# Performance work log

Hardware: AMD Instinct MI355X
Metric: run time of the kernel (lower is better)

Reference implementation:

```python
import jax, jax.numpy as jnp
import numpy as np

DECAY = 0.999
EPS = 1e-05
COMMITMENT_COST = 0.25
M, D = 1024, 256
B, H, W = 32, 32, 32


def setup_inputs() -> dict:
    key = jax.random.key(0)
    k1, k2 = jax.random.split(key)
    init_bound = 1.0 / M
    x = jax.random.normal(k1, (B, H, W, D), dtype=jnp.float32)
    embedding = jax.random.uniform(k2, (M, D), dtype=jnp.float32,
                                   minval=-init_bound, maxval=init_bound)
    ema_count = jnp.zeros((M,), dtype=jnp.float32)
    ema_weight = embedding  # buffer initialized as embedding.clone()
    return {"x": x, "embedding": embedding, "ema_count": ema_count,
            "ema_weight": ema_weight}


def reference(x, embedding, ema_count, ema_weight):
    Mn, Dn = embedding.shape
    x_flat = jax.lax.stop_gradient(x).reshape(-1, Dn)          # [N, D]
    N = x_flat.shape[0]

    # (-cdist)^2 == squared euclidean distance; argmin is the same.
    x_sq = jnp.sum(x_flat * x_flat, axis=-1, keepdims=True)    # [N, 1]
    e_sq = jnp.sum(embedding * embedding, axis=-1)             # [M]
    distances = x_sq - 2.0 * (x_flat @ embedding.T) + e_sq[None, :]  # [N, M]
    indices = jnp.argmin(distances, axis=-1)                   # [N]

    quantized = embedding[indices].reshape(x.shape)            # gather

    # one-hot column sums == scatter-add of ones; encodings.T @ x_flat == scatter-add rows
    counts = jnp.zeros((Mn,), x.dtype).at[indices].add(1.0)    # [M]
    dw = jnp.zeros((Mn, Dn), x.dtype).at[indices].add(x_flat)  # [M, D]

    new_count = DECAY * ema_count + (1.0 - DECAY) * counts
    n = jnp.sum(new_count)
    new_count = (new_count + EPS) / (n + Mn * EPS) * n
    new_weight = DECAY * ema_weight + (1.0 - DECAY) * dw
    new_embedding = new_weight / new_count[:, None]

    codebook_loss = jnp.mean((jax.lax.stop_gradient(x) - quantized) ** 2)
    e_latent_loss = jnp.mean((x - jax.lax.stop_gradient(quantized)) ** 2)
    commitment_loss = COMMITMENT_COST * e_latent_loss

    quantized_st = x + jax.lax.stop_gradient(quantized - x)    # straight-through

    avg_probs = counts / N
    perplexity = jnp.exp(-jnp.sum(avg_probs * jnp.log(avg_probs + 1e-10)))

    return (quantized_st, commitment_loss, codebook_loss, perplexity,
            new_embedding, new_count, new_weight)
```

## Files before the change

### kernel.cpp

```cpp
#include <hip/hip_runtime.h>
#include <cfloat>
#include <math.h>

#define N_TOK 32768
#define DIM   256
#define MCODE 1024

typedef unsigned short u16;
typedef unsigned long long u64;
typedef __attribute__((ext_vector_type(8))) _Float16 h16x8;
typedef __attribute__((ext_vector_type(4))) float f32x4;

constexpr float DECAY_ = 0.999f;
constexpr float OMD_   = (float)(1.0 - 0.999);
constexpr float EPS_   = 1e-5f;
constexpr float MEPS_  = (float)(1024 * 1e-5);

constexpr int WS_EH   = 0;
constexpr int WS_ESQ  = 262144;
constexpr int WS_CNTI = 263168;
constexpr int WS_BI   = 264192;
constexpr int WS_LP   = 296960;
constexpr int WS_KEY  = 299008;

constexpr int OUT_Q        = 0;
constexpr int OUT_COMMIT   = 8388608;
constexpr int OUT_CODEBOOK = 8388609;
constexpr int OUT_PERP     = 8388610;
constexpr int OUT_NE       = 8388611;
constexpr int OUT_NC       = 8650755;
constexpr int OUT_NW       = 8651779;

static __device__ __forceinline__ void gl2lds16(const u16* g, char* l) {
    __builtin_amdgcn_global_load_lds(
        (const __attribute__((address_space(1))) unsigned int*)g,
        (__attribute__((address_space(3))) unsigned int*)l, 16, 0, 0);
}
static __device__ __forceinline__ unsigned fmap(float f) {
    unsigned u = __float_as_uint(f);
    return (u & 0x80000000u) ? ~u : (u | 0x80000000u);
}

static __device__ __forceinline__ void load_row8(const float* __restrict__ src,
                                                 int wave_id, int lane,
                                                 float* vv, size_t* o) {
    int rb = wave_id >> 6, kc = (wave_id >> 3) & 7, t = wave_id & 7;
    int row = rb * 128 + t * 16 + (lane & 15);
    int k   = kc * 32 + (lane >> 4) * 8;
    const float* s = &src[row * DIM + k];
    float4 v0 = *(const float4*)s, v1 = *(const float4*)(s + 4);
    vv[0]=v0.x; vv[1]=v0.y; vv[2]=v0.z; vv[3]=v0.w;
    vv[4]=v1.x; vv[5]=v1.y; vv[6]=v1.z; vv[7]=v1.w;
    *o = (size_t)wave_id * 512 + lane * 8;
}
static __device__ __forceinline__ void pack_wave_h16(const float* __restrict__ src,
                                                     u16* __restrict__ dst,
                                                     int wave_id, int lane,
                                                     float scale) {
    float vv[8]; size_t o;
    load_row8(src, wave_id, lane, vv, &o);
    h16x8 hv;
#pragma unroll
    for (int j = 0; j < 8; ++j) hv[j] = (_Float16)(vv[j] * scale);
    *(h16x8*)&dst[o] = hv;
}

__global__ __launch_bounds__(256) void vq_setup(const float* __restrict__ x,
                                                const float* __restrict__ emb,
                                                u16* __restrict__ xh,
                                                u16* __restrict__ eh,
                                                float* __restrict__ esq,
                                                u64* __restrict__ keys,
                                                int* __restrict__ cnti) {
    const int b = blockIdx.x, tid = threadIdx.x;
    const int lane = tid & 63, w = tid >> 6;
    if (b < 4096) { pack_wave_h16(x, xh, b * 4 + w, lane, 1.0f); return; }
    const int p = b - 4096;
    if (p < 128) {
        pack_wave_h16(emb, eh, p * 4 + w, lane, 1024.0f);
    } else if (p < 384) {
        int c = (p - 128) * 4 + w;
        float4 v = *(const float4*)&emb[c * DIM + lane * 4];
        float s = v.x * v.x + v.y * v.y + v.z * v.z + v.w * v.w;
#pragma unroll
        for (int off = 32; off; off >>= 1) s += __shfl_xor(s, off, 64);
        if (lane == 0) esq[c] = s;
    } else if (p < 512) {
        keys[(p - 384) * 256 + tid] = ~0ULL;
    } else {
#pragma unroll
        for (int i = 0; i < 4; ++i) cnti[i * 256 + tid] = 0;
    }
}

__global__ __launch_bounds__(256) void vq_scores_mfma(const u16* __restrict__ xh,
                                                      const u16* __restrict__ eh,
                                                      const float* __restrict__ esq,
                                                      u64* __restrict__ keys) {
    __shared__ __align__(16) char smem[33792];
    const int tid  = threadIdx.x;
    const int lane = tid & 63, w = tid >> 6;
    const int wm = w & 1, wn = w >> 1;
    const int raw = blockIdx.x;
    const int rb = (raw >> 6) * 8 + (raw & 7);
    const int cs = (raw >> 3) & 7;

    const u16* gb0 = xh + (size_t)rb * 32768;
    const u16* gb1 = eh + (size_t)cs * 32768;

    auto STAGE = [&](int KC, char* base) {
#pragma unroll
        for (int j = 0; j < 4; ++j) {
            int t = w * 4 + j;
            int arr = t >> 3, slot = t & 7;
            const u16* g = (arr == 0 ? gb0 : gb1)
                           + KC * 4096 + slot * 512 + lane * 8;
            gl2lds16(g, base + arr * 8192 + slot * 1024);
        }
    };

    f32x4 acc[4][4];
#pragma unroll
    for (int i = 0; i < 4; ++i)
#pragma unroll
        for (int j = 0; j < 4; ++j) acc[i][j] = (f32x4)0.f;

    STAGE(0, smem);
    __syncthreads();

    for (int kc = 0; kc < 8; ++kc) {
        char* cur = smem + (kc & 1) * 16384;
        char* nxt = smem + ((kc + 1) & 1) * 16384;
        if (kc < 7) STAGE(kc + 1, nxt);

        const h16x8* Ah = (const h16x8*)cur;
        const h16x8* Bh = (const h16x8*)(cur + 8192);
        h16x8 ah[4];
#pragma unroll
        for (int tm = 0; tm < 4; ++tm)
            ah[tm] = Ah[(wm * 4 + tm) * 64 + lane];
#pragma unroll
        for (int tn = 0; tn < 4; ++tn) {
            h16x8 bh = Bh[(wn * 4 + tn) * 64 + lane];
#pragma unroll
            for (int tm = 0; tm < 4; ++tm) {
                acc[tm][tn] = __builtin_amdgcn_mfma_f32_16x16x32_f16(ah[tm], bh, acc[tm][tn], 0, 0, 0);
            }
        }
        __syncthreads();
    }

    float* cv = (float*)smem;
    int*   ci = (int*)(smem + 16896);
    const int ln = lane & 15, quad = lane >> 4;
#pragma unroll
    for (int tm = 0; tm < 4; ++tm) {
        float bv[4];
        int   bi[4];
#pragma unroll
        for (int r = 0; r < 4; ++r) { bv[r] = FLT_MAX; bi[r] = 0; }
#pragma unroll
        for (int tn = 0; tn < 4; ++tn) {
            int c = cs * 128 + wn * 64 + tn * 16 + ln;
            float ec = esq[c];
#pragma unroll
            for (int r = 0; r < 4; ++r) {
                float d = fmaf(-0.001953125f, acc[tm][tn][r], ec);
                if (d < bv[r]) { bv[r] = d; bi[r] = c; }
            }
        }
        int row0 = wm * 64 + tm * 16 + quad * 4;
        int slot = wn * 16 + ln;
#pragma unroll
        for (int r = 0; r < 4; ++r) {
            cv[(row0 + r) * 33 + slot] = bv[r];
            ci[(row0 + r) * 33 + slot] = bi[r];
        }
    }
    __syncthreads();
    if (tid < 128) {
        float bv = cv[tid * 33];
        int   bi = ci[tid * 33];
#pragma unroll
        for (int s = 1; s < 32; ++s) {
            float v = cv[tid * 33 + s];
            int  ix = ci[tid * 33 + s];
            if (v < bv || (v == bv && ix < bi)) { bv = v; bi = ix; }
        }
        u64 key = ((u64)fmap(bv) << 32) | (unsigned)bi;
        atomicMin(&keys[rb * 128 + tid], key);
    }
}

__global__ __launch_bounds__(256) void vq_quant(const float* __restrict__ x,
                                                const float* __restrict__ emb,
                                                const u64* __restrict__ keys,
                                                float* __restrict__ outq,
                                                int* __restrict__ cnti,
                                                int* __restrict__ bi_arr,
                                                float* __restrict__ lpart) {
    const int tid = threadIdx.x, lane = tid & 63, w = tid >> 6;
    const float4* x4 = (const float4*)x;
    const float4* e4 = (const float4*)emb;
    float4* o4 = (float4*)outq;
    float lacc = 0.f;
#pragma unroll
    for (int it = 0; it < 4; ++it) {
        int row = blockIdx.x * 16 + it * 4 + w;
        int bi = (int)(unsigned)(keys[row] & 0xffffffffULL);
        if (lane == 0) { atomicAdd(&cnti[bi], 1); bi_arr[row] = bi; }
        float4 xv = x4[row * 64 + lane];
        float4 ev = e4[bi * 64 + lane];
        float4 q;
        q.x = xv.x + (ev.x - xv.x);  q.y = xv.y + (ev.y - xv.y);
        q.z = xv.z + (ev.z - xv.z);  q.w = xv.w + (ev.w - xv.w);
        o4[row * 64 + lane] = q;
        float dx = xv.x - ev.x, dy = xv.y - ev.y, dz = xv.z - ev.z, dwv = xv.w - ev.w;
        lacc += dx * dx + dy * dy + dz * dz + dwv * dwv;
    }
#pragma unroll
    for (int off = 32; off; off >>= 1) lacc += __shfl_xor(lacc, off, 64);
    __shared__ float red[4];
    if (lane == 0) red[w] = lacc;
    __syncthreads();
    if (tid == 0) lpart[blockIdx.x] = red[0] + red[1] + red[2] + red[3];
}

#define MEGA_CAP 6144
__global__ __launch_bounds__(256) void vq_mega(const float* __restrict__ x,
                                               const float* __restrict__ ema_count,
                                               const float* __restrict__ ema_weight,
                                               const int* __restrict__ cnti,
                                               const int* __restrict__ bi_arr,
                                               const float* __restrict__ lpart,
                                               float* __restrict__ out) {
    const int m = blockIdx.x, tid = threadIdx.x;
    __shared__ float fs[256];
    __shared__ int list[MEGA_CAP];
    __shared__ int lcount;

    float rsum = 0.f;
#pragma unroll
    for (int i = 0; i < 4; ++i) rsum += ema_count[tid * 4 + i];
    fs[tid] = rsum;
    if (tid == 0) lcount = 0;
    __syncthreads();
    for (int s = 128; s; s >>= 1) { if (tid < s) fs[tid] += fs[tid + s]; __syncthreads(); }
    const float n = DECAY_ * fs[0] + OMD_ * (float)N_TOK;
    __syncthreads();

    const int4* b4 = (const int4*)bi_arr;
#pragma unroll 4
    for (int i = tid; i < N_TOK / 4; i += 256) {
        int4 v = b4[i];
        if (v.x == m) { int p = atomicAdd(&lcount, 1); if (p < MEGA_CAP) list[p] = 4 * i; }
        if (v.y == m) { int p = atomicAdd(&lcount, 1); if (p < MEGA_CAP) list[p] = 4 * i + 1; }
        if (v.z == m) { int p = atomicAdd(&lcount, 1); if (p < MEGA_CAP) list[p] = 4 * i + 2; }
        if (v.w == m) { int p = atomicAdd(&lcount, 1); if (p < MEGA_CAP) list[p] = 4 * i + 3; }
    }
    __syncthreads();
    const int nm = lcount;
    float dwsum;
    if (nm <= MEGA_CAP) {
        float a0 = 0.f, a1 = 0.f, a2 = 0.f, a3 = 0.f;
        int i = 0;
        for (; i + 4 <= nm; i += 4) {
            a0 += x[list[i]     * DIM + tid];
            a1 += x[list[i + 1] * DIM + tid];
            a2 += x[list[i + 2] * DIM + tid];
            a3 += x[list[i + 3] * DIM + tid];
        }
        for (; i < nm; ++i) a0 += x[list[i] * DIM + tid];
        dwsum = (a0 + a1) + (a2 + a3);
    } else {
        __shared__ int chunk[256];
        float a0 = 0.f;
        for (int base = 0; base < N_TOK; base += 256) {
            __syncthreads();
            chunk[tid] = bi_arr[base + tid];
            __syncthreads();
            for (int j = 0; j < 256; ++j)
                if (chunk[j] == m) a0 += x[(base + j) * DIM + tid];
        }
        dwsum = a0;
    }

    float raw_m = DECAY_ * ema_count[m] + OMD_ * (float)nm;
    float ncm = (raw_m + EPS_) / (n + MEPS_) * n;
    float nw = DECAY_ * ema_weight[m * DIM + tid] + OMD_ * dwsum;
    out[OUT_NW + m * DIM + tid] = nw;
    out[OUT_NE + m * DIM + tid] = nw / ncm;
    if (tid == 0) out[OUT_NC + m] = ncm;

    if (m == 0) {
        float ent = 0.f;
#pragma unroll
        for (int i = 0; i < 4; ++i) {
            float p = (float)cnti[tid * 4 + i] / (float)N_TOK;
            ent += p * logf(p + 1e-10f);
        }
        __syncthreads();
        fs[tid] = ent;
        __syncthreads();
        for (int s = 128; s; s >>= 1) { if (tid < s) fs[tid] += fs[tid + s]; __syncthreads(); }
        float entr = fs[0];
        __syncthreads();
        float ls = 0.f;
#pragma unroll
        for (int k = 0; k < 8; ++k) ls += lpart[tid + 256 * k];
        fs[tid] = ls;
        __syncthreads();
        for (int s = 128; s; s >>= 1) { if (tid < s) fs[tid] += fs[tid + s]; __syncthreads(); }
        if (tid == 0) {
            float mean = fs[0] / (float)(N_TOK * DIM);
            out[OUT_COMMIT]   = 0.25f * mean;
            out[OUT_CODEBOOK] = mean;
            out[OUT_PERP]     = expf(-entr);
        }
    }
}

extern "C" void kernel_launch(void* const* d_in, const int* in_sizes, int n_in,
                              void* d_out, int out_size, void* d_ws, size_t ws_size,
                              hipStream_t stream) {
    const float* x          = (const float*)d_in[0];
    const float* emb        = (const float*)d_in[1];
    const float* ema_count  = (const float*)d_in[2];
    const float* ema_weight = (const float*)d_in[3];
    float* out = (float*)d_out;
    float* wf  = (float*)d_ws;

    u16* xh = (u16*)d_out;
    u16* eh = (u16*)(wf + WS_EH);

    float* esq    = wf + WS_ESQ;
    int*   cnti   = (int*)(wf + WS_CNTI);
    int*   bi_arr = (int*)(wf + WS_BI);
    float* lpart  = wf + WS_LP;
    u64*   keys   = (u64*)(wf + WS_KEY);

    vq_setup<<<4609, 256, 0, stream>>>(x, emb, xh, eh, esq, keys, cnti);
    vq_scores_mfma<<<2048, 256, 0, stream>>>(xh, eh, esq, keys);
    vq_quant<<<2048, 256, 0, stream>>>(x, emb, keys, out, cnti, bi_arr, lpart);
    vq_mega<<<MCODE, 256, 0, stream>>>(x, ema_count, ema_weight, cnti, bi_arr,
                                       lpart, out);
}
```

Measured before the change: 150.7 us.

## Fuse x fp32-to-fp16 conversion into MFMA score kernel, drop pre-pass

Removes the separate pre-pass that converted all of x to fp16 into a scratch buffer. The scores kernel now loads fp32 x rows straight into registers, converts them to fp16 and writes them to LDS, using register prefetching overlapped with the MFMA loop. This saves writing and re-reading a 16 MB fp16 copy. The cost is that each x tile is now read as fp32 by each of the 8 codebook-slice blocks, doubling per-block A-load bytes, and the conversion work is repeated per block.

Measured after the change: 164.7 us. +9.3%, slower.

```diff
diff --git a/kernel.cpp b/kernel.cpp
--- a/kernel.cpp
+++ b/kernel.cpp
@@ -41,41 +41,30 @@
     return (u & 0x80000000u) ? ~u : (u | 0x80000000u);
 }
 
-static __device__ __forceinline__ void load_row8(const float* __restrict__ src,
-                                                 int wave_id, int lane,
-                                                 float* vv, size_t* o) {
+static __device__ __forceinline__ void pack_wave_h16(const float* __restrict__ src,
+                                                     u16* __restrict__ dst,
+                                                     int wave_id, int lane,
+                                                     float scale) {
     int rb = wave_id >> 6, kc = (wave_id >> 3) & 7, t = wave_id & 7;
     int row = rb * 128 + t * 16 + (lane & 15);
     int k   = kc * 32 + (lane >> 4) * 8;
     const float* s = &src[row * DIM + k];
     float4 v0 = *(const float4*)s, v1 = *(const float4*)(s + 4);
-    vv[0]=v0.x; vv[1]=v0.y; vv[2]=v0.z; vv[3]=v0.w;
-    vv[4]=v1.x; vv[5]=v1.y; vv[6]=v1.z; vv[7]=v1.w;
-    *o = (size_t)wave_id * 512 + lane * 8;
-}
-static __device__ __forceinline__ void pack_wave_h16(const float* __restrict__ src,
-                                                     u16* __restrict__ dst,
-                                                     int wave_id, int lane,
-                                                     float scale) {
-    float vv[8]; size_t o;
-    load_row8(src, wave_id, lane, vv, &o);
     h16x8 hv;
-#pragma unroll
-    for (int j = 0; j < 8; ++j) hv[j] = (_Float16)(vv[j] * scale);
-    *(h16x8*)&dst[o] = hv;
-}
-
-__global__ __launch_bounds__(256) void vq_setup(const float* __restrict__ x,
-                                                const float* __restrict__ emb,
-                                                u16* __restrict__ xh,
+    hv[0]=(_Float16)(v0.x*scale); hv[1]=(_Float16)(v0.y*scale);
+    hv[2]=(_Float16)(v0.z*scale); hv[3]=(_Float16)(v0.w*scale);
+    hv[4]=(_Float16)(v1.x*scale); hv[5]=(_Float16)(v1.y*scale);
+    hv[6]=(_Float16)(v1.z*scale); hv[7]=(_Float16)(v1.w*scale);
+    *(h16x8*)&dst[(size_t)wave_id * 512 + lane * 8] = hv;
+}
+
+__global__ __launch_bounds__(256) void vq_setup(const float* __restrict__ emb,
                                                 u16* __restrict__ eh,
                                                 float* __restrict__ esq,
                                                 u64* __restrict__ keys,
                                                 int* __restrict__ cnti) {
-    const int b = blockIdx.x, tid = threadIdx.x;
+    const int p = blockIdx.x, tid = threadIdx.x;
     const int lane = tid & 63, w = tid >> 6;
-    if (b < 4096) { pack_wave_h16(x, xh, b * 4 + w, lane, 1.0f); return; }
-    const int p = b - 4096;
     if (p < 128) {
         pack_wave_h16(emb, eh, p * 4 + w, lane, 1024.0f);
     } else if (p < 384) {
@@ -93,7 +82,7 @@
     }
 }
 
-__global__ __launch_bounds__(256) void vq_scores_mfma(const u16* __restrict__ xh,
+__global__ __launch_bounds__(256) void vq_scores_mfma(const float* __restrict__ x,
                                                       const u16* __restrict__ eh,
                                                       const float* __restrict__ esq,
                                                       u64* __restrict__ keys) {
@@ -104,20 +93,38 @@
     const int raw = blockIdx.x;
     const int rb = (raw >> 6) * 8 + (raw & 7);
     const int cs = (raw >> 3) & 7;
-
-    const u16* gb0 = xh + (size_t)rb * 32768;
+    const int ln16 = lane & 15, q4 = lane >> 4;
+
     const u16* gb1 = eh + (size_t)cs * 32768;
 
-    auto STAGE = [&](int KC, char* base) {
-#pragma unroll
-        for (int j = 0; j < 4; ++j) {
-            int t = w * 4 + j;
-            int arr = t >> 3, slot = t & 7;
-            const u16* g = (arr == 0 ? gb0 : gb1)
-                           + KC * 4096 + slot * 512 + lane * 8;
-            gl2lds16(g, base + arr * 8192 + slot * 1024);
+    const float* as0 = x + ((size_t)(rb * 128 + (2 * w)     * 16 + ln16)) * DIM + q4 * 8;
+    const float* as1 = x + ((size_t)(rb * 128 + (2 * w + 1) * 16 + ln16)) * DIM + q4 * 8;
+
+    float4 a0, a1, a2, a3;
+
+    auto STAGE_B = [&](int KC, char* base) {
+#pragma unroll
+        for (int j = 0; j < 2; ++j) {
+            int slot = w * 2 + j;
+            const u16* g = gb1 + KC * 4096 + slot * 512 + lane * 8;
+            gl2lds16(g, base + 8192 + slot * 1024);
         }
     };
+    auto LOAD_A = [&](int KC) {
+        a0 = *(const float4*)(as0 + KC * 32);
+        a1 = *(const float4*)(as0 + KC * 32 + 4);
+        a2 = *(const float4*)(as1 + KC * 32);
+        a3 = *(const float4*)(as1 + KC * 32 + 4);
+    };
+    auto WRITE_A = [&](char* base) {
+        h16x8 h0, h1;
+        h0[0]=(_Float16)a0.x; h0[1]=(_Float16)a0.y; h0[2]=(_Float16)a0.z; h0[3]=(_Float16)a0.w;
+        h0[4]=(_Float16)a1.x; h0[5]=(_Float16)a1.y; h0[6]=(_Float16)a1.z; h0[7]=(_Float16)a1.w;
+        h1[0]=(_Float16)a2.x; h1[1]=(_Float16)a2.y; h1[2]=(_Float16)a2.z; h1[3]=(_Float16)a2.w;
+        h1[4]=(_Float16)a3.x; h1[5]=(_Float16)a3.y; h1[6]=(_Float16)a3.z; h1[7]=(_Float16)a3.w;
+        *(h16x8*)(base + (2 * w)     * 1024 + lane * 16) = h0;
+        *(h16x8*)(base + (2 * w + 1) * 1024 + lane * 16) = h1;
+    };
 
     f32x4 acc[4][4];
 #pragma unroll
@@ -125,13 +132,15 @@
 #pragma unroll
         for (int j = 0; j < 4; ++j) acc[i][j] = (f32x4)0.f;
 
-    STAGE(0, smem);
+    STAGE_B(0, smem);
+    LOAD_A(0);
+    WRITE_A(smem);
     __syncthreads();
 
     for (int kc = 0; kc < 8; ++kc) {
         char* cur = smem + (kc & 1) * 16384;
         char* nxt = smem + ((kc + 1) & 1) * 16384;
-        if (kc < 7) STAGE(kc + 1, nxt);
+        if (kc < 7) { STAGE_B(kc + 1, nxt); LOAD_A(kc + 1); }
 
         const h16x8* Ah = (const h16x8*)cur;
         const h16x8* Bh = (const h16x8*)(cur + 8192);
@@ -147,12 +156,12 @@
                 acc[tm][tn] = __builtin_amdgcn_mfma_f32_16x16x32_f16(ah[tm], bh, acc[tm][tn], 0, 0, 0);
             }
         }
+        if (kc < 7) WRITE_A(nxt);
         __syncthreads();
     }
 
     float* cv = (float*)smem;
     int*   ci = (int*)(smem + 16896);
-    const int ln = lane & 15, quad = lane >> 4;
 #pragma unroll
     for (int tm = 0; tm < 4; ++tm) {
         float bv[4];
@@ -161,7 +170,7 @@
         for (int r = 0; r < 4; ++r) { bv[r] = FLT_MAX; bi[r] = 0; }
 #pragma unroll
         for (int tn = 0; tn < 4; ++tn) {
-            int c = cs * 128 + wn * 64 + tn * 16 + ln;
+            int c = cs * 128 + wn * 64 + tn * 16 + ln16;
             float ec = esq[c];
 #pragma unroll
             for (int r = 0; r < 4; ++r) {
@@ -169,8 +178,8 @@
                 if (d < bv[r]) { bv[r] = d; bi[r] = c; }
             }
         }
-        int row0 = wm * 64 + tm * 16 + quad * 4;
-        int slot = wn * 16 + ln;
+        int row0 = wm * 64 + tm * 16 + q4 * 4;
+        int slot = wn * 16 + ln16;
 #pragma unroll
         for (int r = 0; r < 4; ++r) {
             cv[(row0 + r) * 33 + slot] = bv[r];
@@ -330,7 +339,6 @@
     float* out = (float*)d_out;
     float* wf  = (float*)d_ws;
 
-    u16* xh = (u16*)d_out;
     u16* eh = (u16*)(wf + WS_EH);
 
     float* esq    = wf + WS_ESQ;
@@ -339,8 +347,8 @@
     float* lpart  = wf + WS_LP;
     u64*   keys   = (u64*)(wf + WS_KEY);
 
-    vq_setup<<<4609, 256, 0, stream>>>(x, emb, xh, eh, esq, keys, cnti);
-    vq_scores_mfma<<<2048, 256, 0, stream>>>(xh, eh, esq, keys);
+    vq_setup<<<513, 256, 0, stream>>>(emb, eh, esq, keys, cnti);
+    vq_scores_mfma<<<2048, 256, 0, stream>>>(x, eh, esq, keys);
     vq_quant<<<2048, 256, 0, stream>>>(x, emb, keys, out, cnti, bi_arr, lpart);
     vq_mega<<<MCODE, 256, 0, stream>>>(x, ema_count, ema_weight, cnti, bi_arr,
                                        lpart, out);
```
